# Kernel optimization log

Measured on AMD Instinct MI355X. Metric: run time of the kernel, lower is better.

Reference implementation:

```python
import jax, jax.numpy as jnp
import numpy as np

B, S, H = 4, 2048, 576
NH, NKV, HD = 9, 3, 64
GROUPS = NH // NKV
ROPE_THETA = 100000.0
MAX_POS = 8192


def _rope_tables():
    inv_freq = 1.0 / (ROPE_THETA ** (jnp.arange(0, HD, 2, dtype=jnp.float32) / HD))
    t = jnp.arange(MAX_POS, dtype=jnp.float32)
    freqs = jnp.outer(t, inv_freq)              # [MAX_POS, HD//2]
    emb = jnp.concatenate([freqs, freqs], axis=-1)  # [MAX_POS, HD]
    return jnp.cos(emb), jnp.sin(emb)


def _rotate_half(x):
    x1, x2 = x[..., : HD // 2], x[..., HD // 2 :]
    return jnp.concatenate([-x2, x1], axis=-1)


def setup_inputs() -> dict:
    key = jax.random.key(0)
    k1, k2, k3, k4, k5 = jax.random.split(key, 5)
    hidden_states = jax.random.normal(k1, (B, S, H), dtype=jnp.float32)
    # causal additive mask [B,1,S,S]: 0 where allowed, large negative above diagonal
    causal = jnp.triu(jnp.ones((S, S), dtype=bool), k=1)
    attention_mask = jnp.where(causal, jnp.float32(-1e9), jnp.float32(0.0))[None, None]
    attention_mask = jnp.broadcast_to(attention_mask, (B, 1, S, S))
    position_ids = jnp.broadcast_to(jnp.arange(S, dtype=jnp.int32)[None, :], (B, S))
    scale = 1.0 / np.sqrt(H)
    Wq = jax.random.normal(k2, (NH * HD, H), dtype=jnp.float32) * scale
    Wk = jax.random.normal(k3, (NKV * HD, H), dtype=jnp.float32) * scale
    Wv = jax.random.normal(k4, (NKV * HD, H), dtype=jnp.float32) * scale
    Wo = jax.random.normal(k5, (H, NH * HD), dtype=jnp.float32) * scale
    return {"hidden_states": hidden_states, "attention_mask": attention_mask,
            "position_ids": position_ids, "Wq": Wq, "Wk": Wk, "Wv": Wv, "Wo": Wo}


def reference(hidden_states, attention_mask, position_ids, Wq, Wk, Wv, Wo):
    bsz, q_len, _ = hidden_states.shape
    cos_cached, sin_cached = _rope_tables()
    # projections (nn.Linear: x @ W.T), reshape to [B, heads, S, HD]
    q = (hidden_states @ Wq.T).reshape(bsz, q_len, NH, HD).transpose(0, 2, 1, 3)
    k = (hidden_states @ Wk.T).reshape(bsz, q_len, NKV, HD).transpose(0, 2, 1, 3)
    v = (hidden_states @ Wv.T).reshape(bsz, q_len, NKV, HD).transpose(0, 2, 1, 3)
    # RoPE: gather cos/sin per position, broadcast over heads
    cos = cos_cached[position_ids][:, None]  # [B,1,S,HD]
    sin = sin_cached[position_ids][:, None]
    q = q * cos + _rotate_half(q) * sin
    k = k * cos + _rotate_half(k) * sin
    # GQA: repeat_interleave kv heads
    k = jnp.repeat(k, GROUPS, axis=1)  # [B,NH,S,HD]
    v = jnp.repeat(v, GROUPS, axis=1)
    scores = jnp.einsum('bhqd,bhkd->bhqk', q, k) / np.sqrt(HD)
    scores = scores + attention_mask
    probs = jax.nn.softmax(scores.astype(jnp.float32), axis=-1).astype(q.dtype)
    attn = jnp.einsum('bhqk,bhkd->bhqd', probs, v)
    attn = attn.transpose(0, 2, 1, 3).reshape(bsz, q_len, NH * HD)
    return attn @ Wo.T
```

## Files before the change

kernel.cpp:

```cpp
#include <hip/hip_runtime.h>
#include <hip/hip_bf16.h>
#include <math.h>

#define Bsz 4
#define Slen 2048
#define Hdim 576
#define NH 9
#define NKV 3
#define HD 64

typedef __bf16 bf16_t;
typedef __bf16 bf16x8 __attribute__((ext_vector_type(8)));
typedef float f32x4 __attribute__((ext_vector_type(4)));
typedef float f32x16 __attribute__((ext_vector_type(16)));
typedef unsigned int u32;
typedef unsigned int u32x4 __attribute__((ext_vector_type(4)));

static __device__ __forceinline__ bf16x8 load_cvt8(const float* __restrict__ src){
  float4 f0 = *reinterpret_cast<const float4*>(src);
  float4 f1 = *reinterpret_cast<const float4*>(src + 4);
  bf16x8 v;
  v[0]=(bf16_t)f0.x; v[1]=(bf16_t)f0.y; v[2]=(bf16_t)f0.z; v[3]=(bf16_t)f0.w;
  v[4]=(bf16_t)f1.x; v[5]=(bf16_t)f1.y; v[6]=(bf16_t)f1.z; v[7]=(bf16_t)f1.w;
  return v;
}

static __device__ __forceinline__ void gload16(const bf16_t* g, bf16_t* l){
  __builtin_amdgcn_global_load_lds((const __attribute__((address_space(1))) void*)g,
                                   (__attribute__((address_space(3))) void*)l, 16, 0, 0);
}

static __device__ __forceinline__ float xhalf_max(float x){
  return fmaxf(x, __shfl_xor(x, 32, 64));
}
static __device__ __forceinline__ float xhalf_sum(float x){
  return x + __shfl_xor(x, 32, 64);
}

__global__ void setup_kernel(const float* __restrict__ X,
                             const float* __restrict__ Wq,
                             const float* __restrict__ Wk,
                             const float* __restrict__ Wv,
                             const float* __restrict__ Wo,
                             bf16_t* __restrict__ Xb,
                             bf16_t* __restrict__ Wb,
                             bf16_t* __restrict__ Wob,
                             float* __restrict__ cost,
                             float* __restrict__ sint)
{
  const int bid = blockIdx.x;
  if (bid < 256){
    int i = bid * 256 + threadIdx.x;
    int j = i & 31;
    int p = i >> 5;
    double invf = pow(100000.0, -(double)j / 32.0);
    double ang = (double)p * invf;
    cost[i] = (float)cos(ang);
    sint[i] = (float)sin(ang);
    return;
  }
  const int NX  = 8192 * 576 / 8;
  const int NWq = 576 * 576 / 8;
  const int NWk = 192 * 576 / 8;
  int i = (bid - 256) * 256 + threadIdx.x;
  const int total = NX + NWq + 2 * NWk + NWq;
  if (i >= total) return;
  const float* src; bf16_t* dst; int off;
  if (i < NX)                    { src = X;  dst = Xb;            off = i; }
  else if (i < NX + NWq)         { src = Wq; dst = Wb;            off = i - NX; }
  else if (i < NX + NWq + NWk)   { src = Wk; dst = Wb + 331776;   off = i - NX - NWq; }
  else if (i < NX + NWq + 2*NWk) { src = Wv; dst = Wb + 442368;   off = i - NX - NWq - NWk; }
  else                           { src = Wo; dst = Wob;           off = i - NX - NWq - 2*NWk; }
  *reinterpret_cast<bf16x8*>(dst + (size_t)off * 8) = load_cvt8(src + (size_t)off * 8);
}

__launch_bounds__(256)
__global__ void qkv_gemm_kernel(const bf16_t* __restrict__ Xb,
                                const bf16_t* __restrict__ Wb,
                                const int* __restrict__ pos_ids,
                                const float* __restrict__ cost,
                                const float* __restrict__ sint,
                                float qscale,
                                bf16_t* __restrict__ qbuf,
                                bf16_t* __restrict__ kbuf,
                                bf16_t* __restrict__ vtbuf)
{
  __shared__ bf16_t Ald[2][128 * 64];
  __shared__ bf16_t Bld[2][64 * 64];
  const int t = threadIdx.x, l = t & 63, w = t >> 6;
  const int wm = w >> 1, wn = w & 1;
  const int lane16 = l & 15, grp = l >> 4;
  const int m0 = blockIdx.x * 128;
  const int nt = blockIdx.y;
  const int nrow0 = nt * 64;

  const int sr = l >> 3;
  const int sc = ((l & 7) ^ sr) * 8;

  f32x4 acc[4][2];
  #pragma unroll
  for (int mi = 0; mi < 4; ++mi)
    #pragma unroll
    for (int ni = 0; ni < 2; ++ni)
      acc[mi][ni] = (f32x4){0.f, 0.f, 0.f, 0.f};

  auto STAGE = [&](int kt, int buf){
    const int k0 = kt * 64;
    #pragma unroll
    for (int u = 0; u < 4; ++u)
      gload16(Xb + (size_t)(m0 + w * 32 + u * 8 + sr) * Hdim + k0 + sc,
              &Ald[buf][(w * 32 + u * 8) * 64]);
    #pragma unroll
    for (int u = 0; u < 2; ++u)
      gload16(Wb + (size_t)(nrow0 + w * 16 + u * 8 + sr) * Hdim + k0 + sc,
              &Bld[buf][(w * 16 + u * 8) * 64]);
  };

  STAGE(0, 0);
  asm volatile("s_waitcnt vmcnt(0)" ::: "memory");
  __syncthreads();

  const int sl7 = lane16 & 7;
  for (int kt = 0; kt < 9; ++kt){
    const int buf = kt & 1;
    if (kt + 1 < 9) STAGE(kt + 1, buf ^ 1);
    #pragma unroll
    for (int ks = 0; ks < 2; ++ks){
      bf16x8 a[4], bb[2];
      #pragma unroll
      for (int mi = 0; mi < 4; ++mi){
        int row = wm * 64 + mi * 16 + lane16;
        a[mi] = *reinterpret_cast<const bf16x8*>(&Ald[buf][row * 64 + (((ks * 4 + grp) ^ sl7) * 8)]);
      }
      #pragma unroll
      for (int ni = 0; ni < 2; ++ni){
        int row = ni * 32 + wn * 16 + lane16;
        bb[ni] = *reinterpret_cast<const bf16x8*>(&Bld[buf][row * 64 + (((ks * 4 + grp) ^ sl7) * 8)]);
      }
      #pragma unroll
      for (int mi = 0; mi < 4; ++mi)
        #pragma unroll
        for (int ni = 0; ni < 2; ++ni)
          acc[mi][ni] = __builtin_amdgcn_mfma_f32_16x16x32_bf16(a[mi], bb[ni], acc[mi][ni], 0, 0, 0);
    }
    if (kt + 1 < 9){
      asm volatile("s_waitcnt vmcnt(0)" ::: "memory");
      __syncthreads();
    }
  }

  const int d = wn * 16 + lane16;
  #pragma unroll
  for (int mi = 0; mi < 4; ++mi){
    #pragma unroll
    for (int j = 0; j < 4; ++j){
      int m = m0 + wm * 64 + mi * 16 + grp * 4 + j;
      int b = m >> 11;
      int s = m & 2047;
      float x0 = acc[mi][0][j], x1 = acc[mi][1][j];
      if (nt < 12){
        int pos = pos_ids[b * Slen + s];
        float c = cost[pos * 32 + d], sn = sint[pos * 32 + d];
        float scale = (nt < 9) ? qscale : 1.0f;
        float o0 = (x0 * c - x1 * sn) * scale;
        float o1 = (x1 * c + x0 * sn) * scale;
        x0 = o0; x1 = o1;
      }
      if (nt < 9){
        bf16_t* dst = qbuf + (((size_t)b * NH + nt) * Slen + s) * HD;
        dst[d] = (bf16_t)x0; dst[d + 32] = (bf16_t)x1;
      } else if (nt < 12){
        bf16_t* dst = kbuf + (((size_t)b * NKV + (nt - 9)) * Slen + s) * HD;
        dst[d] = (bf16_t)x0; dst[d + 32] = (bf16_t)x1;
      } else {
        bf16_t* dst = vtbuf + ((size_t)b * NKV + (nt - 12)) * HD * Slen + s;
        dst[(size_t)d * Slen] = (bf16_t)x0; dst[(size_t)(d + 32) * Slen] = (bf16_t)x1;
      }
    }
  }
}

__launch_bounds__(128)
__global__ void flash_attn_kernel(const bf16_t* __restrict__ qbuf,
                                  const bf16_t* __restrict__ kbuf,
                                  const bf16_t* __restrict__ vtbuf,
                                  bf16_t* __restrict__ attn_out,
                                  u32* __restrict__ part_O,
                                  float* __restrict__ part_ml)
{
  __shared__ bf16_t Kld[3][32 * 64];
  __shared__ bf16_t Vld[3][64 * 32];
  const int t = threadIdx.x, l = t & 63, w = t >> 6;
  const int l32 = l & 31, hi = l >> 5;

  const int flat = blockIdx.x;
  const int v = flat / 36;
  const int bh = flat % 36;
  int qt, t0, t1, seg;
  if (v < 16){ qt = 16 + v; t0 = 0; t1 = 32; seg = 0; }
  else {
    int i = (v - 16) >> 1;
    if (((v - 16) & 1) == 0){ qt = 15 - i; t0 = 0; t1 = 2 * qt + 2; seg = -1; }
    else                    { qt = 31 - i; t0 = 32; t1 = 2 * qt + 2; seg = 1; }
  }
  const int b = bh / NH, h = bh % NH, kvh = h / (NH / NKV);

  const bf16_t* qp = qbuf + ((size_t)b * NH + h) * Slen * HD;
  const bf16_t* kp = kbuf + ((size_t)b * NKV + kvh) * Slen * HD;
  const bf16_t* vp = vtbuf + ((size_t)b * NKV + kvh) * HD * Slen;

  const int krow = l >> 3;
  const int ksc  = ((l & 7) ^ krow) * 8;
  const int vrow = l >> 2;
  const int vsc  = ((l & 3) ^ ((vrow >> 1) & 3)) * 8;

  auto STAGE = [&](int kt, int buf){
    const int k0 = kt * 32;
    #pragma unroll
    for (int u = 0; u < 2; ++u){
      int ub = w * 2 + u;
      gload16(kp + (size_t)(k0 + ub * 8 + krow) * HD + ksc, &Kld[buf][ub * 512]);
    }
    #pragma unroll
    for (int u = 0; u < 2; ++u){
      int ub = w * 2 + u;
      gload16(vp + (size_t)(ub * 16 + vrow) * Slen + k0 + vsc, &Vld[buf][ub * 512]);
    }
  };

  const int q0 = qt * 64 + w * 32;
  bf16x8 aq[4];
  #pragma unroll
  for (int ds = 0; ds < 4; ++ds)
    aq[ds] = *reinterpret_cast<const bf16x8*>(qp + (size_t)(q0 + l32) * HD + ds * 16 + hi * 8);

  STAGE(t0, 0);
  if (t0 + 1 < t1) STAGE(t0 + 1, 1);

  f32x16 acco[2];
  #pragma unroll
  for (int db = 0; db < 2; ++db)
    #pragma unroll
    for (int r = 0; r < 16; ++r) acco[db][r] = 0.f;
  float mrun = -1e30f, lrun = 0.f;

  int cur = 0;
  const int dt = 2 * qt + w;
  for (int kb = t0; kb < t1; ++kb){
    const bool rem1 = (kb + 1 < t1), rem2 = (kb + 2 < t1);

    if (rem1) asm volatile("s_waitcnt vmcnt(6)" ::: "memory");
    else      asm volatile("s_waitcnt vmcnt(2)" ::: "memory");
    __syncthreads();

    if (rem2){
      int sb = cur + 2; if (sb >= 3) sb -= 3;
      STAGE(kb + 2, sb);
    }

    f32x16 sacc;
    if (kb <= dt){
      #pragma unroll
      for (int r = 0; r < 16; ++r) sacc[r] = 0.f;
      __builtin_amdgcn_s_setprio(1);
      #pragma unroll
      for (int ds = 0; ds < 4; ++ds){
        bf16x8 ak = *reinterpret_cast<const bf16x8*>(
            &Kld[cur][l32 * 64 + (((ds * 2 + hi) ^ (l32 & 7)) * 8)]);
        sacc = __builtin_amdgcn_mfma_f32_32x32x16_bf16(ak, aq[ds], sacc, 0, 0, 0);
      }
      __builtin_amdgcn_s_setprio(0);

      if (kb == dt){
        #pragma unroll
        for (int r = 0; r < 16; ++r){
          int crow = (r & 3) + 8 * (r >> 2) + 4 * hi;
          if (crow > l32) sacc[r] = -1e30f;
        }
      }

      float m0_ = fmaxf(sacc[0], sacc[1]),  m1_ = fmaxf(sacc[2], sacc[3]);
      float m2_ = fmaxf(sacc[4], sacc[5]),  m3_ = fmaxf(sacc[6], sacc[7]);
      float m4_ = fmaxf(sacc[8], sacc[9]),  m5_ = fmaxf(sacc[10], sacc[11]);
      float m6_ = fmaxf(sacc[12], sacc[13]), m7_ = fmaxf(sacc[14], sacc[15]);
      m0_ = fmaxf(m0_, m1_); m2_ = fmaxf(m2_, m3_); m4_ = fmaxf(m4_, m5_); m6_ = fmaxf(m6_, m7_);
      float tmax = fmaxf(fmaxf(m0_, m2_), fmaxf(m4_, m6_));
      tmax = xhalf_max(tmax);

      if (__ballot(tmax - mrun > 8.f)){
        float mnew = fmaxf(mrun, tmax);
        float sf = __builtin_amdgcn_exp2f(mrun - mnew);
        lrun *= sf;
        #pragma unroll
        for (int db = 0; db < 2; ++db)
          #pragma unroll
          for (int r = 0; r < 16; ++r) acco[db][r] *= sf;
        mrun = mnew;
      }

      #pragma unroll
      for (int r = 0; r < 16; ++r)
        sacc[r] = __builtin_amdgcn_exp2f(sacc[r] - mrun);
      float s0 = sacc[0] + sacc[1],  s1 = sacc[2] + sacc[3];
      float s2 = sacc[4] + sacc[5],  s3 = sacc[6] + sacc[7];
      float s4 = sacc[8] + sacc[9],  s5 = sacc[10] + sacc[11];
      float s6 = sacc[12] + sacc[13], s7 = sacc[14] + sacc[15];
      s0 += s1; s2 += s3; s4 += s5; s6 += s7;
      float rsum = (s0 + s2) + (s4 + s6);
      lrun += xhalf_sum(rsum);
    }

    u32x4 pa0, pa1;
    if (kb <= dt){
      u32 wv[8];
      #pragma unroll
      for (int j = 0; j < 8; ++j){
        float lo = sacc[2 * j], hp = sacc[2 * j + 1];
        asm("v_cvt_pk_bf16_f32 %0, %1, %2" : "=v"(wv[j]) : "v"(lo), "v"(hp));
      }
      asm volatile("v_permlane32_swap_b32 %0, %1" : "+v"(wv[0]), "+v"(wv[2]));
      asm volatile("v_permlane32_swap_b32 %0, %1" : "+v"(wv[1]), "+v"(wv[3]));
      asm volatile("v_permlane32_swap_b32 %0, %1" : "+v"(wv[4]), "+v"(wv[6]));
      asm volatile("v_permlane32_swap_b32 %0, %1" : "+v"(wv[5]), "+v"(wv[7]));
      pa0 = (u32x4){wv[0], wv[1], wv[2], wv[3]};
      pa1 = (u32x4){wv[4], wv[5], wv[6], wv[7]};
    }

    if (rem2)      asm volatile("s_waitcnt vmcnt(8)" ::: "memory");
    else if (rem1) asm volatile("s_waitcnt vmcnt(4)" ::: "memory");
    else           asm volatile("s_waitcnt vmcnt(0)" ::: "memory");
    __syncthreads();

    if (kb <= dt){
      __builtin_amdgcn_s_setprio(1);
      #pragma unroll
      for (int ks = 0; ks < 2; ++ks){
        #pragma unroll
        for (int db = 0; db < 2; ++db){
          bf16x8 av = *reinterpret_cast<const bf16x8*>(
              &Vld[cur][(db * 32 + l32) * 32 + (((ks * 2 + hi) ^ ((l32 >> 1) & 3)) * 8)]);
          acco[db] = __builtin_amdgcn_mfma_f32_32x32x16_bf16(
              av, __builtin_bit_cast(bf16x8, ks ? pa1 : pa0), acco[db], 0, 0, 0);
        }
      }
      __builtin_amdgcn_s_setprio(0);
    }

    cur = (cur + 1 == 3) ? 0 : cur + 1;
  }

  if (seg < 0){
    const float linv = 1.0f / lrun;
    const int srow = q0 + l32;
    bf16_t* orow = attn_out + ((size_t)b * Slen + srow) * (NH * HD) + h * HD;
    #pragma unroll
    for (int db = 0; db < 2; ++db){
      #pragma unroll
      for (int j = 0; j < 8; ++j){
        int r = 2 * j;
        int d = db * 32 + (r & 3) + 8 * (r >> 2) + 4 * hi;
        u32 pw;
        float lo = acco[db][r] * linv, hp = acco[db][r + 1] * linv;
        asm("v_cvt_pk_bf16_f32 %0, %1, %2" : "=v"(pw) : "v"(lo), "v"(hp));
        *reinterpret_cast<u32*>(orow + d) = pw;
      }
    }
  } else {
    const int slot = (bh * 16 + (qt - 16)) * 2 + seg;
    u32* po = part_O + ((size_t)slot * 2 + w) * 1024;
    float* pml = part_ml + ((size_t)slot * 2 + w) * 64;
    #pragma unroll
    for (int db = 0; db < 2; ++db){
      #pragma unroll
      for (int j = 0; j < 8; ++j){
        int r = 2 * j;
        int d = db * 32 + (r & 3) + 8 * (r >> 2) + 4 * hi;
        u32 pw;
        float lo = acco[db][r], hp = acco[db][r + 1];
        asm("v_cvt_pk_bf16_f32 %0, %1, %2" : "=v"(pw) : "v"(lo), "v"(hp));
        po[(d >> 1) * 32 + l32] = pw;
      }
    }
    if (hi == 0){ pml[l32] = mrun; pml[32 + l32] = lrun; }
  }
}

__launch_bounds__(128)
__global__ void combine_kernel(const u32* __restrict__ part_O,
                               const float* __restrict__ part_ml,
                               bf16_t* __restrict__ attn_out)
{
  const int idx = blockIdx.x;
  const int bh = idx % 36, qtm = idx / 36;
  const int qt = 16 + qtm;
  const int b = bh / NH, h = bh % NH;
  const int t = threadIdx.x;
  const int q = t & 31, wg = (t >> 5) & 1, half = t >> 6;
  const int slot0 = (bh * 16 + qtm) * 2;

  const float* pml0 = part_ml + ((size_t)(slot0 + 0) * 2 + wg) * 64;
  const float* pml1 = part_ml + ((size_t)(slot0 + 1) * 2 + wg) * 64;
  float m1 = pml0[q], l1 = pml0[32 + q];
  float m2 = pml1[q], l2 = pml1[32 + q];
  float m = fmaxf(m1, m2);
  float a1 = __builtin_amdgcn_exp2f(m1 - m);
  float a2 = __builtin_amdgcn_exp2f(m2 - m);
  float linv = 1.0f / (l1 * a1 + l2 * a2);
  a1 *= linv; a2 *= linv;

  const u32* po0 = part_O + ((size_t)(slot0 + 0) * 2 + wg) * 1024;
  const u32* po1 = part_O + ((size_t)(slot0 + 1) * 2 + wg) * 1024;
  const int s = qt * 64 + wg * 32 + q;
  bf16_t* orow = attn_out + ((size_t)b * Slen + s) * (NH * HD) + h * HD;

  #pragma unroll
  for (int u = 0; u < 16; ++u){
    int dp = half * 16 + u;
    u32 v1 = po0[dp * 32 + q], v2 = po1[dp * 32 + q];
    float lo = a1 * __builtin_bit_cast(float, v1 << 16)
             + a2 * __builtin_bit_cast(float, v2 << 16);
    float hv = a1 * __builtin_bit_cast(float, v1 & 0xffff0000u)
             + a2 * __builtin_bit_cast(float, v2 & 0xffff0000u);
    u32 pw;
    asm("v_cvt_pk_bf16_f32 %0, %1, %2" : "=v"(pw) : "v"(lo), "v"(hv));
    *reinterpret_cast<u32*>(orow + 2 * dp) = pw;
  }
}

__launch_bounds__(256)
__global__ void out_gemm_kernel(const bf16_t* __restrict__ A,
                                const bf16_t* __restrict__ Wob,
                                float* __restrict__ out)
{
  __shared__ bf16_t Ald[2][128 * 64];
  __shared__ bf16_t Bld[2][64 * 64];
  const int t = threadIdx.x, l = t & 63, w = t >> 6;
  const int wm = w >> 1, wn = w & 1;
  const int lane16 = l & 15, grp = l >> 4;
  const int m0 = blockIdx.x * 128;
  const int nt = blockIdx.y;
  const int nrow0 = nt * 64;

  const int sr = l >> 3;
  const int sc = ((l & 7) ^ sr) * 8;

  f32x4 acc[4][2];
  #pragma unroll
  for (int mi = 0; mi < 4; ++mi)
    #pragma unroll
    for (int ni = 0; ni < 2; ++ni)
      acc[mi][ni] = (f32x4){0.f, 0.f, 0.f, 0.f};

  auto STAGE = [&](int kt, int buf){
    const int k0 = kt * 64;
    #pragma unroll
    for (int u = 0; u < 4; ++u)
      gload16(A + (size_t)(m0 + w * 32 + u * 8 + sr) * Hdim + k0 + sc,
              &Ald[buf][(w * 32 + u * 8) * 64]);
    #pragma unroll
    for (int u = 0; u < 2; ++u)
      gload16(Wob + (size_t)(nrow0 + w * 16 + u * 8 + sr) * Hdim + k0 + sc,
              &Bld[buf][(w * 16 + u * 8) * 64]);
  };

  STAGE(0, 0);
  asm volatile("s_waitcnt vmcnt(0)" ::: "memory");
  __syncthreads();

  const int sl7 = lane16 & 7;
  for (int kt = 0; kt < 9; ++kt){
    const int buf = kt & 1;
    if (kt + 1 < 9) STAGE(kt + 1, buf ^ 1);
    #pragma unroll
    for (int ks = 0; ks < 2; ++ks){
      bf16x8 a[4], bb[2];
      #pragma unroll
      for (int mi = 0; mi < 4; ++mi){
        int row = wm * 64 + mi * 16 + lane16;
        a[mi] = *reinterpret_cast<const bf16x8*>(&Ald[buf][row * 64 + (((ks * 4 + grp) ^ sl7) * 8)]);
      }
      #pragma unroll
      for (int ni = 0; ni < 2; ++ni){
        int row = wn * 32 + ni * 16 + lane16;
        bb[ni] = *reinterpret_cast<const bf16x8*>(&Bld[buf][row * 64 + (((ks * 4 + grp) ^ sl7) * 8)]);
      }
      #pragma unroll
      for (int mi = 0; mi < 4; ++mi)
        #pragma unroll
        for (int ni = 0; ni < 2; ++ni)
          acc[mi][ni] = __builtin_amdgcn_mfma_f32_16x16x32_bf16(a[mi], bb[ni], acc[mi][ni], 0, 0, 0);
    }
    if (kt + 1 < 9){
      asm volatile("s_waitcnt vmcnt(0)" ::: "memory");
      __syncthreads();
    }
  }

  #pragma unroll
  for (int mi = 0; mi < 4; ++mi){
    #pragma unroll
    for (int ni = 0; ni < 2; ++ni){
      #pragma unroll
      for (int j = 0; j < 4; ++j){
        int m = m0 + wm * 64 + mi * 16 + grp * 4 + j;
        int n = nrow0 + wn * 32 + ni * 16 + lane16;
        out[(size_t)m * Hdim + n] = acc[mi][ni][j];
      }
    }
  }
}

extern "C" void kernel_launch(void* const* d_in, const int* in_sizes, int n_in,
                              void* d_out, int out_size, void* d_ws, size_t ws_size,
                              hipStream_t stream) {
  const float* X   = (const float*)d_in[0];
  const int* pos   = (const int*)d_in[2];
  const float* Wq  = (const float*)d_in[3];
  const float* Wk  = (const float*)d_in[4];
  const float* Wv  = (const float*)d_in[5];
  const float* Wo  = (const float*)d_in[6];
  float* out = (float*)d_out;

  char* ws = (char*)d_ws;
  float* cost = (float*)ws;
  float* sint = (float*)(ws + 262144);
  bf16_t* qb  = (bf16_t*)(ws + 524288);
  bf16_t* kb  = qb + (size_t)Bsz * NH * Slen * HD;
  bf16_t* vt  = kb + (size_t)Bsz * NKV * Slen * HD;
  bf16_t* Xb  = vt + (size_t)Bsz * NKV * Slen * HD;
  bf16_t* ab  = Xb;
  bf16_t* Wb  = Xb + (size_t)8192 * 576;
  bf16_t* Wob = Wb + (size_t)960 * 576;
  u32*  part_O  = (u32*)(Wob + (size_t)576 * 576);
  float* part_ml = (float*)(part_O + (size_t)1152 * 2 * 1024);

  const float QSCALE = 0.125f * 1.44269504088896f;

  setup_kernel<<<dim3(256 + 2736), dim3(256), 0, stream>>>(X, Wq, Wk, Wv, Wo, Xb, Wb, Wob, cost, sint);
  qkv_gemm_kernel<<<dim3(64, 15), dim3(256), 0, stream>>>(Xb, Wb, pos, cost, sint, QSCALE, qb, kb, vt);
  flash_attn_kernel<<<dim3(1728), dim3(128), 0, stream>>>(qb, kb, vt, ab, part_O, part_ml);
  combine_kernel<<<dim3(576), dim3(128), 0, stream>>>(part_O, part_ml, ab);
  out_gemm_kernel<<<dim3(64, 9), dim3(256), 0, stream>>>(ab, Wob, out);
}
```

Before: 119.5 us.

## Split every query tile into two equal KV halves and double-buffer K/V staging

The flash-attention work split changes from a mixed scheme (full tiles for upper query tiles, split tiles for some) to a uniform one. Every query tile is now split into two equal KV segments, giving 2304 blocks that all write partials, and the combine kernel merges all 32 query tiles. The K/V LDS ring shrinks from triple to double buffering, with the next stage issued after an extra barrier at the end of each iteration. This aims to balance per-block work and cut LDS footprint, at the cost of more partial-output traffic, a larger combine pass and less prefetch overlap.

```diff
diff --git a/kernel.cpp b/kernel.cpp
--- a/kernel.cpp
+++ b/kernel.cpp
@@ -184,25 +184,21 @@
 __global__ void flash_attn_kernel(const bf16_t* __restrict__ qbuf,
                                   const bf16_t* __restrict__ kbuf,
                                   const bf16_t* __restrict__ vtbuf,
-                                  bf16_t* __restrict__ attn_out,
                                   u32* __restrict__ part_O,
                                   float* __restrict__ part_ml)
 {
-  __shared__ bf16_t Kld[3][32 * 64];
-  __shared__ bf16_t Vld[3][64 * 32];
+  __shared__ bf16_t Kld[2][32 * 64];
+  __shared__ bf16_t Vld[2][64 * 32];
   const int t = threadIdx.x, l = t & 63, w = t >> 6;
   const int l32 = l & 31, hi = l >> 5;
 
   const int flat = blockIdx.x;
   const int v = flat / 36;
   const int bh = flat % 36;
-  int qt, t0, t1, seg;
-  if (v < 16){ qt = 16 + v; t0 = 0; t1 = 32; seg = 0; }
-  else {
-    int i = (v - 16) >> 1;
-    if (((v - 16) & 1) == 0){ qt = 15 - i; t0 = 0; t1 = 2 * qt + 2; seg = -1; }
-    else                    { qt = 31 - i; t0 = 32; t1 = 2 * qt + 2; seg = 1; }
-  }
+  const int qt = 31 - (v >> 1);
+  const int seg = v & 1;
+  const int t0 = seg * (qt + 1);
+  const int t1 = t0 + qt + 1;
   const int b = bh / NH, h = bh % NH, kvh = h / (NH / NKV);
 
   const bf16_t* qp = qbuf + ((size_t)b * NH + h) * Slen * HD;
@@ -244,19 +240,14 @@
     for (int r = 0; r < 16; ++r) acco[db][r] = 0.f;
   float mrun = -1e30f, lrun = 0.f;
 
-  int cur = 0;
   const int dt = 2 * qt + w;
   for (int kb = t0; kb < t1; ++kb){
+    const int cur = (kb - t0) & 1;
     const bool rem1 = (kb + 1 < t1), rem2 = (kb + 2 < t1);
 
     if (rem1) asm volatile("s_waitcnt vmcnt(6)" ::: "memory");
     else      asm volatile("s_waitcnt vmcnt(2)" ::: "memory");
     __syncthreads();
-
-    if (rem2){
-      int sb = cur + 2; if (sb >= 3) sb -= 3;
-      STAGE(kb + 2, sb);
-    }
 
     f32x16 sacc;
     if (kb <= dt){
@@ -326,9 +317,8 @@
       pa1 = (u32x4){wv[4], wv[5], wv[6], wv[7]};
     }
 
-    if (rem2)      asm volatile("s_waitcnt vmcnt(8)" ::: "memory");
-    else if (rem1) asm volatile("s_waitcnt vmcnt(4)" ::: "memory");
-    else           asm volatile("s_waitcnt vmcnt(0)" ::: "memory");
+    if (rem1) asm volatile("s_waitcnt vmcnt(4)" ::: "memory");
+    else      asm volatile("s_waitcnt vmcnt(0)" ::: "memory");
     __syncthreads();
 
     if (kb <= dt){
@@ -346,43 +336,28 @@
       __builtin_amdgcn_s_setprio(0);
     }
 
-    cur = (cur + 1 == 3) ? 0 : cur + 1;
-  }
-
-  if (seg < 0){
-    const float linv = 1.0f / lrun;
-    const int srow = q0 + l32;
-    bf16_t* orow = attn_out + ((size_t)b * Slen + srow) * (NH * HD) + h * HD;
-    #pragma unroll
-    for (int db = 0; db < 2; ++db){
-      #pragma unroll
-      for (int j = 0; j < 8; ++j){
-        int r = 2 * j;
-        int d = db * 32 + (r & 3) + 8 * (r >> 2) + 4 * hi;
-        u32 pw;
-        float lo = acco[db][r] * linv, hp = acco[db][r + 1] * linv;
-        asm("v_cvt_pk_bf16_f32 %0, %1, %2" : "=v"(pw) : "v"(lo), "v"(hp));
-        *reinterpret_cast<u32*>(orow + d) = pw;
-      }
-    }
-  } else {
-    const int slot = (bh * 16 + (qt - 16)) * 2 + seg;
-    u32* po = part_O + ((size_t)slot * 2 + w) * 1024;
-    float* pml = part_ml + ((size_t)slot * 2 + w) * 64;
-    #pragma unroll
-    for (int db = 0; db < 2; ++db){
-      #pragma unroll
-      for (int j = 0; j < 8; ++j){
-        int r = 2 * j;
-        int d = db * 32 + (r & 3) + 8 * (r >> 2) + 4 * hi;
-        u32 pw;
-        float lo = acco[db][r], hp = acco[db][r + 1];
-        asm("v_cvt_pk_bf16_f32 %0, %1, %2" : "=v"(pw) : "v"(lo), "v"(hp));
-        po[(d >> 1) * 32 + l32] = pw;
-      }
-    }
-    if (hi == 0){ pml[l32] = mrun; pml[32 + l32] = lrun; }
-  }
+    if (rem2){
+      __syncthreads();
+      STAGE(kb + 2, cur);
+    }
+  }
+
+  const int slot = (bh * 32 + qt) * 2 + seg;
+  u32* po = part_O + ((size_t)slot * 2 + w) * 1024;
+  float* pml = part_ml + ((size_t)slot * 2 + w) * 64;
+  #pragma unroll
+  for (int db = 0; db < 2; ++db){
+    #pragma unroll
+    for (int j = 0; j < 8; ++j){
+      int r = 2 * j;
+      int d = db * 32 + (r & 3) + 8 * (r >> 2) + 4 * hi;
+      u32 pw;
+      float lo = acco[db][r], hp = acco[db][r + 1];
+      asm("v_cvt_pk_bf16_f32 %0, %1, %2" : "=v"(pw) : "v"(lo), "v"(hp));
+      po[(d >> 1) * 32 + l32] = pw;
+    }
+  }
+  if (hi == 0){ pml[l32] = mrun; pml[32 + l32] = lrun; }
 }
 
 __launch_bounds__(128)
@@ -391,12 +366,11 @@
                                bf16_t* __restrict__ attn_out)
 {
   const int idx = blockIdx.x;
-  const int bh = idx % 36, qtm = idx / 36;
-  const int qt = 16 + qtm;
+  const int bh = idx % 36, qt = idx / 36;
   const int b = bh / NH, h = bh % NH;
   const int t = threadIdx.x;
   const int q = t & 31, wg = (t >> 5) & 1, half = t >> 6;
-  const int slot0 = (bh * 16 + qtm) * 2;
+  const int slot0 = (bh * 32 + qt) * 2;
 
   const float* pml0 = part_ml + ((size_t)(slot0 + 0) * 2 + wg) * 64;
   const float* pml1 = part_ml + ((size_t)(slot0 + 1) * 2 + wg) * 64;
@@ -532,13 +506,13 @@
   bf16_t* Wb  = Xb + (size_t)8192 * 576;
   bf16_t* Wob = Wb + (size_t)960 * 576;
   u32*  part_O  = (u32*)(Wob + (size_t)576 * 576);
-  float* part_ml = (float*)(part_O + (size_t)1152 * 2 * 1024);
+  float* part_ml = (float*)(part_O + (size_t)2304 * 2 * 1024);
 
   const float QSCALE = 0.125f * 1.44269504088896f;
 
   setup_kernel<<<dim3(256 + 2736), dim3(256), 0, stream>>>(X, Wq, Wk, Wv, Wo, Xb, Wb, Wob, cost, sint);
   qkv_gemm_kernel<<<dim3(64, 15), dim3(256), 0, stream>>>(Xb, Wb, pos, cost, sint, QSCALE, qb, kb, vt);
-  flash_attn_kernel<<<dim3(1728), dim3(128), 0, stream>>>(qb, kb, vt, ab, part_O, part_ml);
-  combine_kernel<<<dim3(576), dim3(128), 0, stream>>>(part_O, part_ml, ab);
+  flash_attn_kernel<<<dim3(2304), dim3(128), 0, stream>>>(qb, kb, vt, part_O, part_ml);
+  combine_kernel<<<dim3(1152), dim3(128), 0, stream>>>(part_O, part_ml, ab);
   out_gemm_kernel<<<dim3(64, 9), dim3(256), 0, stream>>>(ab, Wob, out);
 }
```

Result: no change. 117.9 us (-1.3%).
